# Kernel tuning notes

Measured on AMD Instinct MI355X. Metric: run time of the kernel, lower is better.

The kernel has to match this reference:

```python
import jax, jax.numpy as jnp
import numpy as np

B, C = 16, 1024
EPS = 1e-12
TINY = 1e-9


def setup_inputs() -> dict:
    key = jax.random.key(0)
    k1, k2 = jax.random.split(key)
    lower = jax.random.normal(k1, (B, C), dtype=jnp.float32)
    # guarantee upper >= lower as required by bound propagation
    upper = lower + jax.random.uniform(k2, (B, C), dtype=jnp.float32)
    return {"lower": lower, "upper": upper}


def reference(lower, upper):
    l, u = lower, upper
    Bv, Cv = l.shape
    eye = jnp.eye(Cv, dtype=l.dtype)          # (C,C)
    offdiag = 1.0 - eye                        # zero on diagonal

    # pairwise logit differences d_ij = x_j - x_i, bounded by [l_d, u_d]; diag forced to 0
    l_d = (l[:, None, :] - u[:, :, None]) * offdiag   # (B,C,C)
    u_d = (u[:, None, :] - l[:, :, None]) * offdiag   # (B,C,C)

    exp_l = jnp.exp(l_d)
    exp_u = jnp.exp(u_d)

    # exp upper bound: secant over [l_d, u_d]
    denom = u_d - l_d
    a_u = (exp_u - exp_l) / (denom + EPS)
    a_u = jnp.where(jnp.abs(denom) < TINY, exp_u, a_u)
    b_u = exp_l - a_u * l_d

    # exp lower bound: tangent at midpoint t
    t = 0.5 * (l_d + u_d)
    a_l = jnp.exp(t)
    b_l = a_l - a_l * t                        # exp(t) - a_l * t

    # zero diagonal entries (i == j term excluded from the sum)
    a_u = a_u * offdiag
    b_u = b_u * offdiag
    a_l = a_l * offdiag
    b_l = b_l * offdiag
    exp_l_od = exp_l * offdiag
    exp_u_od = exp_u * offdiag

    S_l = exp_l_od.sum(axis=2)                 # (B,C)
    S_u = exp_u_od.sum(axis=2)                 # (B,C)

    # linear coefficients of S_i w.r.t. logits x: off-diag from a, diag collects -sum_j a_ij
    sum_a_u = a_u.sum(axis=2)                  # (B,C)
    sum_a_l = a_l.sum(axis=2)
    coef_S_upper = a_u - eye[None, :, :] * sum_a_u[:, :, None]
    coef_S_lower = a_l - eye[None, :, :] * sum_a_l[:, :, None]
    bias_S_upper = b_u.sum(axis=2)
    bias_S_lower = b_l.sum(axis=2)

    # g(S) = 1 / (1 + S), decreasing & convex
    g_at_S_l = 1.0 / (1.0 + S_l)
    g_at_S_u = 1.0 / (1.0 + S_u)

    # upper relaxation of g: tangent (secant of decreasing convex fn swaps roles)
    denom_g = S_u - S_l
    m_u = (g_at_S_u - g_at_S_l) / (denom_g + EPS)
    m_u = jnp.where(jnp.abs(denom_g) < TINY, -1.0 / (1.0 + S_u) ** 2, m_u)
    c_u = g_at_S_l - m_u * S_l

    # lower relaxation of g: tangent at S_u
    m_l = -1.0 / (1.0 + S_u) ** 2
    c_l = 1.0 / (1.0 + S_u) - m_l * S_u

    # compose (m_u >= ... careful with sign handled as in original: direct product)
    final_upper_coef = m_u[:, :, None] * coef_S_upper   # (B,C,C)
    final_lower_coef = m_l[:, :, None] * coef_S_lower   # (B,C,C)
    final_upper_bias = m_u * bias_S_upper + c_u          # (B,C)
    final_lower_bias = m_l * bias_S_lower + c_l          # (B,C)

    soft_lower = jnp.clip(g_at_S_u, 0.0, 1.0)
    soft_upper = jnp.clip(g_at_S_l, 0.0, 1.0)

    return (soft_lower, soft_upper,
            final_lower_coef, final_upper_coef,
            final_lower_bias, final_upper_bias)
```

## Files before the change

### kernel.cpp

```cpp
#include <hip/hip_runtime.h>

namespace {

constexpr int B = 16;
constexpr int C = 1024;
constexpr int BC = B * C;
constexpr long long BCC = (long long)B * C * C;
constexpr float EPS  = 1e-12f;
constexpr float TINY = 1e-9f;

__global__ __launch_bounds__(256) void bounded_softmax_kernel(
    const float* __restrict__ lower,
    const float* __restrict__ upper,
    float* __restrict__ out)
{
    const int row = blockIdx.x;
    const int b   = row >> 10;
    const int i   = row & (C - 1);
    const int tid = threadIdx.x;

    const float* __restrict__ lrow = lower + b * C;
    const float* __restrict__ urow = upper + b * C;

    const float l_i = lrow[i];
    const float u_i = urow[i];

    const float4 lj4 = *reinterpret_cast<const float4*>(lrow + tid * 4);
    const float4 uj4 = *reinterpret_cast<const float4*>(urow + tid * 4);
    const float ljv[4] = {lj4.x, lj4.y, lj4.z, lj4.w};
    const float ujv[4] = {uj4.x, uj4.y, uj4.z, uj4.w};

    float a_u[4], a_l[4];
    float acc[6] = {0.f, 0.f, 0.f, 0.f, 0.f, 0.f};

    #pragma unroll
    for (int k = 0; k < 4; ++k) {
        const int j = tid * 4 + k;
        const float l_d = ljv[k] - u_i;
        const float u_d = ujv[k] - l_i;
        const float el  = __expf(l_d);
        const float eu  = __expf(u_d);
        const float denom = u_d - l_d;
        float au = (eu - el) / (denom + EPS);
        au = (fabsf(denom) < TINY) ? eu : au;
        const float bu = fmaf(-au, l_d, el);
        const float t  = 0.5f * (l_d + u_d);
        const float al = __expf(t);
        const float bl = al * (1.0f - t);

        float elz = el, euz = eu, auz = au, buz = bu, alz = al, blz = bl;
        if (j == i) { elz = euz = auz = buz = alz = blz = 0.0f; }

        acc[0] += elz; acc[1] += euz; acc[2] += auz;
        acc[3] += alz; acc[4] += buz; acc[5] += blz;
        a_u[k] = auz; a_l[k] = alz;
    }

    __shared__ float red[4][6];
    const int lane = tid & 63;
    const int wid  = tid >> 6;
    #pragma unroll
    for (int m = 0; m < 6; ++m) {
        float v = acc[m];
        #pragma unroll
        for (int o = 32; o > 0; o >>= 1) v += __shfl_down(v, o);
        if (lane == 0) red[wid][m] = v;
    }
    __syncthreads();

    const float S_l  = red[0][0] + red[1][0] + red[2][0] + red[3][0];
    const float S_u  = red[0][1] + red[1][1] + red[2][1] + red[3][1];
    const float SA_u = red[0][2] + red[1][2] + red[2][2] + red[3][2];
    const float SA_l = red[0][3] + red[1][3] + red[2][3] + red[3][3];
    const float SB_u = red[0][4] + red[1][4] + red[2][4] + red[3][4];
    const float SB_l = red[0][5] + red[1][5] + red[2][5] + red[3][5];

    const float g_l = 1.0f / (1.0f + S_l);
    const float g_u = 1.0f / (1.0f + S_u);
    const float dg  = S_u - S_l;
    float m_u = (g_u - g_l) / (dg + EPS);
    m_u = (fabsf(dg) < TINY) ? (-g_u * g_u) : m_u;
    const float c_u = g_l - m_u * S_l;
    const float m_l = -g_u * g_u;
    const float c_l = g_u - m_l * S_u;

    float* __restrict__ lower_coef = out + 2 * BC + (long long)row * C;
    float* __restrict__ upper_coef = out + 2 * BC + BCC + (long long)row * C;

    float lv[4], uv[4];
    #pragma unroll
    for (int k = 0; k < 4; ++k) {
        const int j = tid * 4 + k;
        const float dl = (j == i) ? SA_l : 0.0f;
        const float du = (j == i) ? SA_u : 0.0f;
        lv[k] = m_l * (a_l[k] - dl);
        uv[k] = m_u * (a_u[k] - du);
    }
    *reinterpret_cast<float4*>(lower_coef + tid * 4) =
        make_float4(lv[0], lv[1], lv[2], lv[3]);
    *reinterpret_cast<float4*>(upper_coef + tid * 4) =
        make_float4(uv[0], uv[1], uv[2], uv[3]);

    if (tid == 0) {
        const float soft_lower = fminf(fmaxf(g_u, 0.0f), 1.0f);
        const float soft_upper = fminf(fmaxf(g_l, 0.0f), 1.0f);
        out[row]                          = soft_lower;
        out[BC + row]                     = soft_upper;
        out[2 * BC + 2 * BCC + row]       = fmaf(m_l, SB_l, c_l);
        out[2 * BC + 2 * BCC + BC + row]  = fmaf(m_u, SB_u, c_u);
    }
}

}

extern "C" void kernel_launch(void* const* d_in, const int* in_sizes, int n_in,
                              void* d_out, int out_size, void* d_ws, size_t ws_size,
                              hipStream_t stream) {
    const float* lower = (const float*)d_in[0];
    const float* upper = (const float*)d_in[1];
    float* out = (float*)d_out;
    bounded_softmax_kernel<<<dim3(B * C), dim3(256), 0, stream>>>(lower, upper, out);
}
```

Before: 151.0 us.

## Factor exponentials per row and process eight rows per block

Rewrites the pairwise exp terms as products of per-element exponentials (exp(x_j)·exp(-x_i)), so the sums over j of exp_l, exp_u and the tangent terms become batch-wide reductions computed once per block. Only the secant slope needs a per-row reduction. Each block now handles 8 rows, uses a fast reciprocal in place of division, and writes outputs with nontemporal stores. This cuts exp and division work and the number of reductions, at the cost of possible overflow or precision differences from the factorised exponentials and less block-level parallelism.

```diff
diff --git a/kernel.cpp b/kernel.cpp
--- a/kernel.cpp
+++ b/kernel.cpp
@@ -8,106 +8,143 @@
 constexpr long long BCC = (long long)B * C * C;
 constexpr float EPS  = 1e-12f;
 constexpr float TINY = 1e-9f;
+constexpr int TI = 8;
+
+using f32x4 = __attribute__((ext_vector_type(4))) float;
 
 __global__ __launch_bounds__(256) void bounded_softmax_kernel(
     const float* __restrict__ lower,
     const float* __restrict__ upper,
     float* __restrict__ out)
 {
-    const int row = blockIdx.x;
-    const int b   = row >> 10;
-    const int i   = row & (C - 1);
     const int tid = threadIdx.x;
+    constexpr int rowsPerBatch = C / TI;
+    const int b  = blockIdx.x / rowsPerBatch;
+    const int i0 = (blockIdx.x % rowsPerBatch) * TI;
 
     const float* __restrict__ lrow = lower + b * C;
     const float* __restrict__ urow = upper + b * C;
 
-    const float l_i = lrow[i];
-    const float u_i = urow[i];
-
-    const float4 lj4 = *reinterpret_cast<const float4*>(lrow + tid * 4);
-    const float4 uj4 = *reinterpret_cast<const float4*>(urow + tid * 4);
-    const float ljv[4] = {lj4.x, lj4.y, lj4.z, lj4.w};
-    const float ujv[4] = {uj4.x, uj4.y, uj4.z, uj4.w};
-
-    float a_u[4], a_l[4];
-    float acc[6] = {0.f, 0.f, 0.f, 0.f, 0.f, 0.f};
-
+    const f32x4 lj4 = *reinterpret_cast<const f32x4*>(lrow + tid * 4);
+    const f32x4 uj4 = *reinterpret_cast<const f32x4*>(urow + tid * 4);
+    float lk[4], wk[4], El[4], Eu[4], Em[4];
+    float s0 = 0.f, s1 = 0.f, s2 = 0.f, s3 = 0.f;
     #pragma unroll
     for (int k = 0; k < 4; ++k) {
-        const int j = tid * 4 + k;
-        const float l_d = ljv[k] - u_i;
-        const float u_d = ujv[k] - l_i;
-        const float el  = __expf(l_d);
-        const float eu  = __expf(u_d);
-        const float denom = u_d - l_d;
-        float au = (eu - el) / (denom + EPS);
-        au = (fabsf(denom) < TINY) ? eu : au;
-        const float bu = fmaf(-au, l_d, el);
-        const float t  = 0.5f * (l_d + u_d);
-        const float al = __expf(t);
-        const float bl = al * (1.0f - t);
-
-        float elz = el, euz = eu, auz = au, buz = bu, alz = al, blz = bl;
-        if (j == i) { elz = euz = auz = buz = alz = blz = 0.0f; }
-
-        acc[0] += elz; acc[1] += euz; acc[2] += auz;
-        acc[3] += alz; acc[4] += buz; acc[5] += blz;
-        a_u[k] = auz; a_l[k] = alz;
+        const float lj = lj4[k];
+        const float uj = uj4[k];
+        lk[k] = lj;
+        wk[k] = uj - lj;
+        El[k] = __expf(lj);
+        Eu[k] = __expf(uj);
+        const float mk = 0.5f * (lj + uj);
+        Em[k] = __expf(mk);
+        s0 += El[k]; s1 += Eu[k]; s2 += Em[k]; s3 += mk * Em[k];
     }
 
-    __shared__ float red[4][6];
+    __shared__ float red0[4][4];
+    __shared__ float bs[4];
+    __shared__ float red[2][4][2];
     const int lane = tid & 63;
     const int wid  = tid >> 6;
     #pragma unroll
-    for (int m = 0; m < 6; ++m) {
-        float v = acc[m];
-        #pragma unroll
-        for (int o = 32; o > 0; o >>= 1) v += __shfl_down(v, o);
-        if (lane == 0) red[wid][m] = v;
+    for (int o = 32; o > 0; o >>= 1) {
+        s0 += __shfl_down(s0, o);
+        s1 += __shfl_down(s1, o);
+        s2 += __shfl_down(s2, o);
+        s3 += __shfl_down(s3, o);
+    }
+    if (lane == 0) {
+        red0[wid][0] = s0; red0[wid][1] = s1;
+        red0[wid][2] = s2; red0[wid][3] = s3;
     }
     __syncthreads();
+    if (tid < 4)
+        bs[tid] = red0[0][tid] + red0[1][tid] + red0[2][tid] + red0[3][tid];
+    __syncthreads();
+    const float SEl = bs[0], SEu = bs[1], SEm = bs[2], SmEm = bs[3];
 
-    const float S_l  = red[0][0] + red[1][0] + red[2][0] + red[3][0];
-    const float S_u  = red[0][1] + red[1][1] + red[2][1] + red[3][1];
-    const float SA_u = red[0][2] + red[1][2] + red[2][2] + red[3][2];
-    const float SA_l = red[0][3] + red[1][3] + red[2][3] + red[3][3];
-    const float SB_u = red[0][4] + red[1][4] + red[2][4] + red[3][4];
-    const float SB_l = red[0][5] + red[1][5] + red[2][5] + red[3][5];
+    for (int r = 0; r < TI; ++r) {
+        const int i = i0 + r;
+        const float l_i = lrow[i];
+        const float u_i = urow[i];
+        const float w_i = u_i - l_i;
+        const float m_i = 0.5f * (l_i + u_i);
+        const float e_li = __expf(-l_i);
+        const float e_ui = __expf(-u_i);
+        const float e_mi = __expf(-m_i);
+        const float ewp  = __expf(w_i);
+        const float ewn  = __expf(-w_i);
 
-    const float g_l = 1.0f / (1.0f + S_l);
-    const float g_u = 1.0f / (1.0f + S_u);
-    const float dg  = S_u - S_l;
-    float m_u = (g_u - g_l) / (dg + EPS);
-    m_u = (fabsf(dg) < TINY) ? (-g_u * g_u) : m_u;
-    const float c_u = g_l - m_u * S_l;
-    const float m_l = -g_u * g_u;
-    const float c_l = g_u - m_l * S_u;
+        const float S_l  = fmaf(e_ui, SEl, -ewn);
+        const float S_u  = fmaf(e_li, SEu, -ewp);
+        const float SA_l = fmaf(e_mi, SEm, -1.0f);
+        const float SB_l = SA_l - e_mi * SmEm + m_i * e_mi * SEm;
 
-    float* __restrict__ lower_coef = out + 2 * BC + (long long)row * C;
-    float* __restrict__ upper_coef = out + 2 * BC + BCC + (long long)row * C;
+        float au[4];
+        float ra = 0.f, rb = 0.f;
+        #pragma unroll
+        for (int k = 0; k < 4; ++k) {
+            const float eu    = Eu[k] * e_li;
+            const float el    = El[k] * e_ui;
+            const float denom = wk[k] + w_i;
+            float a = (eu - el) * __builtin_amdgcn_rcpf(denom + EPS);
+            a = (fabsf(denom) < TINY) ? eu : a;
+            au[k] = a;
+            const float l_d = lk[k] - u_i;
+            ra += a;
+            rb = fmaf(a, l_d, rb);
+        }
+        #pragma unroll
+        for (int o = 32; o > 0; o >>= 1) {
+            ra += __shfl_down(ra, o);
+            rb += __shfl_down(rb, o);
+        }
+        const int p = r & 1;
+        if (lane == 0) { red[p][wid][0] = ra; red[p][wid][1] = rb; }
+        __syncthreads();
+        const float sa_full = red[p][0][0] + red[p][1][0] + red[p][2][0] + red[p][3][0];
+        const float sb_full = red[p][0][1] + red[p][1][1] + red[p][2][1] + red[p][3][1];
 
-    float lv[4], uv[4];
-    #pragma unroll
-    for (int k = 0; k < 4; ++k) {
-        const int j = tid * 4 + k;
-        const float dl = (j == i) ? SA_l : 0.0f;
-        const float du = (j == i) ? SA_u : 0.0f;
-        lv[k] = m_l * (a_l[k] - dl);
-        uv[k] = m_u * (a_u[k] - du);
-    }
-    *reinterpret_cast<float4*>(lower_coef + tid * 4) =
-        make_float4(lv[0], lv[1], lv[2], lv[3]);
-    *reinterpret_cast<float4*>(upper_coef + tid * 4) =
-        make_float4(uv[0], uv[1], uv[2], uv[3]);
+        const float dden = w_i + w_i;
+        float a_d = (ewp - ewn) * __builtin_amdgcn_rcpf(dden + EPS);
+        a_d = (fabsf(dden) < TINY) ? ewp : a_d;
+        const float SA_u  = sa_full - a_d;
+        const float SBu2  = sb_full + a_d * w_i;
+        const float SB_u  = S_l - SBu2;
 
-    if (tid == 0) {
-        const float soft_lower = fminf(fmaxf(g_u, 0.0f), 1.0f);
-        const float soft_upper = fminf(fmaxf(g_l, 0.0f), 1.0f);
-        out[row]                          = soft_lower;
-        out[BC + row]                     = soft_upper;
-        out[2 * BC + 2 * BCC + row]       = fmaf(m_l, SB_l, c_l);
-        out[2 * BC + 2 * BCC + BC + row]  = fmaf(m_u, SB_u, c_u);
+        const float g_l = 1.0f / (1.0f + S_l);
+        const float g_u = 1.0f / (1.0f + S_u);
+        const float dg  = S_u - S_l;
+        float m_u = (g_u - g_l) / (dg + EPS);
+        m_u = (fabsf(dg) < TINY) ? (-g_u * g_u) : m_u;
+        const float c_u = g_l - m_u * S_l;
+        const float m_l = -g_u * g_u;
+        const float c_l = g_u - m_l * S_u;
+
+        const int row = b * C + i;
+        float* __restrict__ lower_coef = out + 2 * BC + (long long)row * C;
+        float* __restrict__ upper_coef = out + 2 * BC + BCC + (long long)row * C;
+
+        const float Kl = m_l * e_mi;
+        const float dl = -m_l * SA_l;
+        const float du = -m_u * SA_u;
+        f32x4 lv, uv;
+        #pragma unroll
+        for (int k = 0; k < 4; ++k) {
+            const int j = tid * 4 + k;
+            lv[k] = (j == i) ? dl : Kl * Em[k];
+            uv[k] = (j == i) ? du : m_u * au[k];
+        }
+        __builtin_nontemporal_store(lv, reinterpret_cast<f32x4*>(lower_coef + tid * 4));
+        __builtin_nontemporal_store(uv, reinterpret_cast<f32x4*>(upper_coef + tid * 4));
+
+        if (tid == 0) {
+            out[row]                         = fminf(fmaxf(g_u, 0.f), 1.f);
+            out[BC + row]                    = fminf(fmaxf(g_l, 0.f), 1.f);
+            out[2 * BC + 2 * BCC + row]      = fmaf(m_l, SB_l, c_l);
+            out[2 * BC + 2 * BCC + BC + row] = fmaf(m_u, SB_u, c_u);
+        }
     }
 }
 
@@ -119,5 +156,5 @@
     const float* lower = (const float*)d_in[0];
     const float* upper = (const float*)d_in[1];
     float* out = (float*)d_out;
-    bounded_softmax_kernel<<<dim3(B * C), dim3(256), 0, stream>>>(lower, upper, out);
+    bounded_softmax_kernel<<<dim3(BC / TI), dim3(256), 0, stream>>>(lower, upper, out);
 }
```

Result: faster. 145.5 us (-3.6%).
